# Kernel tuning notes

Hardware: AMD Instinct MI355X
Metric: run time of the kernel (lower is better)

The kernel has to match this reference:

```python
import jax, jax.numpy as jnp
import numpy as np

HIDDEN = 2048
NUM_HEADS = 16
HEAD_DIM = HIDDEN // NUM_HEADS
HARMONICS = 64


def _holo_params(key, in_features, out_features, harmonics):
    kb, kp = jax.random.split(key)
    basis = jax.random.normal(kb, (harmonics, in_features), dtype=jnp.float32)
    basis = basis / jnp.linalg.norm(basis, axis=1, keepdims=True)  # F.normalize(p=2, dim=1)
    phase = jax.random.normal(kp, (out_features, harmonics), dtype=jnp.float32) * 0.1
    amp = jnp.ones((out_features, harmonics), dtype=jnp.float32) / np.sqrt(harmonics).astype(np.float32)
    return basis, phase, amp


def setup_inputs() -> dict:
    key = jax.random.key(0)
    ks = jax.random.split(key, 5)
    hidden_states = jax.random.normal(ks[0], (2, 2048, HIDDEN), dtype=jnp.float32)
    inp = {"hidden_states": hidden_states}
    for name, k in zip(("q", "k", "v", "o"), ks[1:]):
        basis, phase, amp = _holo_params(k, HIDDEN, HIDDEN, HARMONICS)
        inp[f"basis_{name}"] = basis
        inp[f"phase_{name}"] = phase
        inp[f"amp_{name}"] = amp
    return inp


def _holo_linear(x, basis, phase, amp):
    # resonance: (B,S,H) = x @ basis^T; modulated-sum == resonance @ (amp*cos(phase))^T
    resonance = jnp.einsum('bsd,hd->bsh', x, basis)
    w = amp * jnp.cos(phase)  # (out, harmonics)
    return jnp.einsum('bsh,oh->bso', resonance, w)


def reference(hidden_states, basis_q, phase_q, amp_q, basis_k, phase_k, amp_k,
              basis_v, phase_v, amp_v, basis_o, phase_o, amp_o):
    bsz, seq_len, _ = hidden_states.shape
    q = _holo_linear(hidden_states, basis_q, phase_q, amp_q)
    k = _holo_linear(hidden_states, basis_k, phase_k, amp_k)
    v = _holo_linear(hidden_states, basis_v, phase_v, amp_v)
    # (B, H, S, Dh)
    q = q.reshape(bsz, seq_len, NUM_HEADS, HEAD_DIM).transpose(0, 2, 1, 3)
    k = k.reshape(bsz, seq_len, NUM_HEADS, HEAD_DIM).transpose(0, 2, 1, 3)
    v = v.reshape(bsz, seq_len, NUM_HEADS, HEAD_DIM).transpose(0, 2, 1, 3)
    scale = 1.0 / np.sqrt(HEAD_DIM).astype(np.float32)
    scores = jnp.einsum('bhqd,bhkd->bhqk', q, k) * scale
    attn = jax.nn.softmax(scores, axis=-1)
    out = jnp.einsum('bhqk,bhkd->bhqd', attn, v)
    out = out.transpose(0, 2, 1, 3).reshape(bsz, seq_len, HIDDEN)
    return _holo_linear(out, basis_o, phase_o, amp_o)
```

## Files before the change

### kernel.cpp

```cpp
#include <hip/hip_runtime.h>
#include <hip/hip_bf16.h>
#include <math.h>

#define HIDDEN 2048
#define HARM   64
#define NHEADS 16
#define HDIM   128
#define SEQ    2048
#define BATCH  2
#define ROWS   (BATCH*SEQ)
#define RN     (ROWS*HARM)
#define PN     ((size_t)ROWS*HIDDEN)

using bf16x8 = __attribute__((ext_vector_type(8))) short;
using f32x16 = __attribute__((ext_vector_type(16))) float;
using u32x2  = __attribute__((ext_vector_type(2))) unsigned;

#if defined(__has_builtin)
#if __has_builtin(__builtin_amdgcn_exp2f)
#define EXP2F(x) __builtin_amdgcn_exp2f(x)
#else
#define EXP2F(x) exp2f(x)
#endif
#else
#define EXP2F(x) exp2f(x)
#endif

#if defined(__has_builtin) && __has_builtin(__builtin_amdgcn_permlane32_swap)
__device__ inline void plane_swap_u(unsigned& a, unsigned& b) {
  u32x2 r = __builtin_amdgcn_permlane32_swap(a, b, false, false);
  a = r[0]; b = r[1];
}
__device__ inline void plane_swap_f(float& a, float& b) {
  union { float f; unsigned u; } ua, ub;
  ua.f = a; ub.f = b;
  u32x2 r = __builtin_amdgcn_permlane32_swap(ua.u, ub.u, false, false);
  ua.u = r[0]; ub.u = r[1];
  a = ua.f; b = ub.f;
}
#else
__device__ inline void plane_swap_u(unsigned& a, unsigned& b) {
  const bool hi = (threadIdx.x & 32) != 0;
  unsigned ax = (unsigned)__shfl_xor((int)a, 32);
  unsigned bx = (unsigned)__shfl_xor((int)b, 32);
  unsigned r0 = hi ? bx : a;
  unsigned r1 = hi ? b : ax;
  a = r0; b = r1;
}
__device__ inline void plane_swap_f(float& a, float& b) {
  const bool hi = (threadIdx.x & 32) != 0;
  float ax = __shfl_xor(a, 32);
  float bx = __shfl_xor(b, 32);
  float r0 = hi ? bx : a;
  float r1 = hi ? b : ax;
  a = r0; b = r1;
}
#endif

__device__ inline void split_bf(float a, ushort& hi, ushort& lo) {
  __hip_bfloat16 h = __float2bfloat16(a);
  float hf = __bfloat162float(h);
  __hip_bfloat16 l = __float2bfloat16(a - hf);
  union { __hip_bfloat16 b; ushort u; } c1, c2;
  c1.b = h; c2.b = l;
  hi = c1.u; lo = c2.u;
}

__global__ __launch_bounds__(256) void prep(
    const float* __restrict__ X,
    const float* __restrict__ pq, const float* __restrict__ aq,
    const float* __restrict__ pk, const float* __restrict__ ak,
    const float* __restrict__ pv, const float* __restrict__ av,
    const float* __restrict__ po, const float* __restrict__ ao,
    const float* __restrict__ bq, const float* __restrict__ bk,
    const float* __restrict__ bv, const float* __restrict__ bo,
    ushort* __restrict__ Xh, ushort* __restrict__ Xl,
    ushort* __restrict__ Wh, ushort* __restrict__ Wl,
    ushort* __restrict__ Bh, ushort* __restrict__ Bl) {
  const int bid = blockIdx.x;
  const int t = threadIdx.x;
  if (bid < 8192) {
    size_t i = ((size_t)bid * 256 + t) * 4;
    float4 v = *(const float4*)&X[i];
    ushort4 h, l;
    split_bf(v.x, h.x, l.x); split_bf(v.y, h.y, l.y);
    split_bf(v.z, h.z, l.z); split_bf(v.w, h.w, l.w);
    *(ushort4*)&Xh[i] = h;
    *(ushort4*)&Xl[i] = l;
  } else if (bid < 10240) {
    int i = (bid - 8192) * 256 + t;
    const int N = HIDDEN * HARM;
    int set = i / N, j = i - set * N;
    const float* p = (set == 0) ? pq : (set == 1) ? pk : (set == 2) ? pv : po;
    const float* a = (set == 0) ? aq : (set == 1) ? ak : (set == 2) ? av : ao;
    float wv = a[j] * cosf(p[j]);
    ushort h, l;
    split_bf(wv, h, l);
    size_t o = (size_t)set * N + j;
    Wh[o] = h; Wl[o] = l;
  } else {
    int idx = bid - 10240;
    int z = idx >> 7, xb = idx & 127;
    const float* S = (z == 0) ? bq : (z == 1) ? bk : (z == 2) ? bv : bo;
    size_t i = ((size_t)xb * 256 + t) * 4;
    float4 v = *(const float4*)&S[i];
    ushort4 h, l;
    split_bf(v.x, h.x, l.x); split_bf(v.y, h.y, l.y);
    split_bf(v.z, h.z, l.z); split_bf(v.w, h.w, l.w);
    size_t o = (size_t)z * HARM * HIDDEN + i;
    *(ushort4*)&Bh[o] = h;
    *(ushort4*)&Bl[o] = l;
  }
}

__global__ __launch_bounds__(256) void gemm_res(
    const ushort* __restrict__ Xh, const ushort* __restrict__ Xl,
    const ushort* __restrict__ Bh, const ushort* __restrict__ Bl,
    float* __restrict__ R0, float* __restrict__ R1, float* __restrict__ R2) {
  const int z = blockIdx.z;
  const ushort* Bhz = Bh + (size_t)z * HARM * HIDDEN;
  const ushort* Blz = Bl + (size_t)z * HARM * HIDDEN;
  float* Rp = (z == 0) ? R0 : (z == 1) ? R1 : R2;
  const int row0 = blockIdx.x * 64;
  const int kc = blockIdx.y;
  __shared__ __align__(16) ushort Xs[2][64][72];
  __shared__ __align__(16) ushort Bs[2][64][72];
  const int t = threadIdx.x;
  const int lane = t & 63, w = t >> 6;
  const int l31 = lane & 31, hh = lane >> 5;
  const int m0 = (w & 1) * 32, n0 = (w >> 1) * 32;
  const int srow = t >> 2;
  const int sc = (t & 3) * 16;
  f32x16 acc;
  #pragma unroll
  for (int j = 0; j < 16; ++j) acc[j] = 0.0f;

  const int kbase = kc * 512;
  for (int k0 = kbase; k0 < kbase + 512; k0 += 64) {
    const size_t xo = (size_t)(row0 + srow) * HIDDEN + k0 + sc;
    const size_t bo = (size_t)srow * HIDDEN + k0 + sc;
    *(uint4*)&Xs[0][srow][sc]     = *(const uint4*)&Xh[xo];
    *(uint4*)&Xs[0][srow][sc + 8] = *(const uint4*)&Xh[xo + 8];
    *(uint4*)&Xs[1][srow][sc]     = *(const uint4*)&Xl[xo];
    *(uint4*)&Xs[1][srow][sc + 8] = *(const uint4*)&Xl[xo + 8];
    *(uint4*)&Bs[0][srow][sc]     = *(const uint4*)&Bhz[bo];
    *(uint4*)&Bs[0][srow][sc + 8] = *(const uint4*)&Bhz[bo + 8];
    *(uint4*)&Bs[1][srow][sc]     = *(const uint4*)&Blz[bo];
    *(uint4*)&Bs[1][srow][sc + 8] = *(const uint4*)&Blz[bo + 8];
    __syncthreads();
    #pragma unroll
    for (int ks = 0; ks < 4; ++ks) {
      bf16x8 ah = *(const bf16x8*)&Xs[0][m0 + l31][ks * 16 + 8 * hh];
      bf16x8 al = *(const bf16x8*)&Xs[1][m0 + l31][ks * 16 + 8 * hh];
      bf16x8 bh = *(const bf16x8*)&Bs[0][n0 + l31][ks * 16 + 8 * hh];
      bf16x8 bl = *(const bf16x8*)&Bs[1][n0 + l31][ks * 16 + 8 * hh];
      acc = __builtin_amdgcn_mfma_f32_32x32x16_bf16(ah, bh, acc, 0, 0, 0);
      acc = __builtin_amdgcn_mfma_f32_32x32x16_bf16(al, bh, acc, 0, 0, 0);
      acc = __builtin_amdgcn_mfma_f32_32x32x16_bf16(ah, bl, acc, 0, 0, 0);
    }
    __syncthreads();
  }
  float* out = Rp + (size_t)kc * ROWS * HARM;
  #pragma unroll
  for (int r = 0; r < 16; ++r) {
    int mloc = (r & 3) + 8 * (r >> 2) + 4 * hh;
    out[(size_t)(row0 + m0 + mloc) * HARM + n0 + l31] = acc[r];
  }
}

__global__ __launch_bounds__(256) void reduce_r(
    const float* __restrict__ R0, const float* __restrict__ R1,
    const float* __restrict__ R2,
    ushort* __restrict__ H0, ushort* __restrict__ L0,
    ushort* __restrict__ H1, ushort* __restrict__ L1,
    ushort* __restrict__ H2, ushort* __restrict__ L2) {
  const int z = blockIdx.y;
  const float* Rp = (z == 0) ? R0 : (z == 1) ? R1 : R2;
  ushort* H = (z == 0) ? H0 : (z == 1) ? H1 : H2;
  ushort* L = (z == 0) ? L0 : (z == 1) ? L1 : L2;
  const size_t i = ((size_t)blockIdx.x * 256 + threadIdx.x) * 8;
  ushort4 h0, l0, h1, l1;
  #pragma unroll
  for (int half = 0; half < 2; ++half) {
    const size_t o = i + half * 4;
    float4 p0 = *(const float4*)&Rp[o];
    float4 p1 = *(const float4*)&Rp[RN + o];
    float4 p2 = *(const float4*)&Rp[2 * (size_t)RN + o];
    float4 p3 = *(const float4*)&Rp[3 * (size_t)RN + o];
    ushort4& hh = half ? h1 : h0;
    ushort4& ll = half ? l1 : l0;
    split_bf(p0.x + p1.x + p2.x + p3.x, hh.x, ll.x);
    split_bf(p0.y + p1.y + p2.y + p3.y, hh.y, ll.y);
    split_bf(p0.z + p1.z + p2.z + p3.z, hh.z, ll.z);
    split_bf(p0.w + p1.w + p2.w + p3.w, hh.w, ll.w);
  }
  *(ushort4*)&H[i] = h0; *(ushort4*)&H[i + 4] = h1;
  *(ushort4*)&L[i] = l0; *(ushort4*)&L[i + 4] = l1;
}

__global__ __launch_bounds__(256) void gemm_proj(
    const ushort* __restrict__ Rh0, const ushort* __restrict__ Rl0,
    const ushort* __restrict__ Rh1, const ushort* __restrict__ Rl1,
    const ushort* __restrict__ Rh2, const ushort* __restrict__ Rl2,
    const ushort* __restrict__ Wh, const ushort* __restrict__ Wl,
    ushort* __restrict__ P0, ushort* __restrict__ P1, ushort* __restrict__ Vt) {
  const int z = blockIdx.z;
  const ushort* Rh = (z == 0) ? Rh0 : (z == 1) ? Rh1 : Rh2;
  const ushort* Rl = (z == 0) ? Rl0 : (z == 1) ? Rl1 : Rl2;
  const ushort* Whz = Wh + (size_t)z * HIDDEN * HARM;
  const ushort* Wlz = Wl + (size_t)z * HIDDEN * HARM;
  const int row0 = blockIdx.x * 32;
  const int col0 = blockIdx.y * 128;
  __shared__ __align__(16) union PSM {
    struct { ushort Rs[2][32][72]; ushort Ws[2][128][72]; } s;
    ushort ct[128][36];
  } sm;
  const int t = threadIdx.x;
  const int lane = t & 63, w = t >> 6;
  const int l31 = lane & 31, hh = lane >> 5;
  {
    const int r = t >> 3, h0 = (t & 7) * 8;
    const size_t o = (size_t)(row0 + r) * HARM + h0;
    *(uint4*)&sm.s.Rs[0][r][h0] = *(const uint4*)&Rh[o];
    *(uint4*)&sm.s.Rs[1][r][h0] = *(const uint4*)&Rl[o];
  }
  #pragma unroll
  for (int i = 0; i < 4; ++i) {
    int idx = t + i * 256;
    int o = idx >> 3, c8 = (idx & 7) * 8;
    const size_t go = (size_t)(col0 + o) * HARM + c8;
    *(uint4*)&sm.s.Ws[0][o][c8] = *(const uint4*)&Whz[go];
    *(uint4*)&sm.s.Ws[1][o][c8] = *(const uint4*)&Wlz[go];
  }
  __syncthreads();
  const int n0 = w * 32;
  f32x16 acc;
  #pragma unroll
  for (int j = 0; j < 16; ++j) acc[j] = 0.0f;
  #pragma unroll
  for (int ks = 0; ks < 4; ++ks) {
    bf16x8 ah = *(const bf16x8*)&sm.s.Rs[0][l31][ks * 16 + 8 * hh];
    bf16x8 al = *(const bf16x8*)&sm.s.Rs[1][l31][ks * 16 + 8 * hh];
    bf16x8 bh = *(const bf16x8*)&sm.s.Ws[0][n0 + l31][ks * 16 + 8 * hh];
    bf16x8 bl = *(const bf16x8*)&sm.s.Ws[1][n0 + l31][ks * 16 + 8 * hh];
    acc = __builtin_amdgcn_mfma_f32_32x32x16_bf16(ah, bh, acc, 0, 0, 0);
    acc = __builtin_amdgcn_mfma_f32_32x32x16_bf16(al, bh, acc, 0, 0, 0);
    acc = __builtin_amdgcn_mfma_f32_32x32x16_bf16(ah, bl, acc, 0, 0, 0);
  }
  if (z < 2) {
    ushort* P = (z == 0) ? P0 : P1;
    #pragma unroll
    for (int r = 0; r < 16; ++r) {
      int mloc = (r & 3) + 8 * (r >> 2) + 4 * hh;
      union { __hip_bfloat16 b; ushort u; } cv;
      cv.b = __float2bfloat16(acc[r]);
      P[(size_t)(row0 + mloc) * HIDDEN + col0 + n0 + l31] = cv.u;
    }
  } else {
    __syncthreads();
    #pragma unroll
    for (int r = 0; r < 16; ++r) {
      int mloc = (r & 3) + 8 * (r >> 2) + 4 * hh;
      union { __hip_bfloat16 b; ushort u; } cv;
      cv.b = __float2bfloat16(acc[r]);
      sm.ct[n0 + l31][mloc] = cv.u;
    }
    __syncthreads();
    if (t < 128) {
      const int batch = row0 >> 11;
      const int tok0 = row0 & 2047;
      ushort* dst = Vt + (size_t)batch * SEQ * HIDDEN +
                    (size_t)(col0 + t) * SEQ + tok0;
      #pragma unroll
      for (int j = 0; j < 4; ++j)
        *(uint4*)&dst[j * 8] = *(const uint4*)&sm.ct[t][j * 8];
    }
  }
}

__global__ __launch_bounds__(256) void gemm_proj_f32(
    const ushort* __restrict__ Rh, const ushort* __restrict__ Rl,
    const ushort* __restrict__ Whz, const ushort* __restrict__ Wlz,
    float* __restrict__ P) {
  const int row0 = blockIdx.x * 32;
  const int col0 = blockIdx.y * 128;
  __shared__ __align__(16) ushort Rs[2][32][72];
  __shared__ __align__(16) ushort Ws[2][128][72];
  const int t = threadIdx.x;
  const int lane = t & 63, w = t >> 6;
  const int l31 = lane & 31, hh = lane >> 5;
  {
    const int r = t >> 3, h0 = (t & 7) * 8;
    const size_t o = (size_t)(row0 + r) * HARM + h0;
    *(uint4*)&Rs[0][r][h0] = *(const uint4*)&Rh[o];
    *(uint4*)&Rs[1][r][h0] = *(const uint4*)&Rl[o];
  }
  #pragma unroll
  for (int i = 0; i < 4; ++i) {
    int idx = t + i * 256;
    int o = idx >> 3, c8 = (idx & 7) * 8;
    const size_t go = (size_t)(col0 + o) * HARM + c8;
    *(uint4*)&Ws[0][o][c8] = *(const uint4*)&Whz[go];
    *(uint4*)&Ws[1][o][c8] = *(const uint4*)&Wlz[go];
  }
  __syncthreads();
  const int n0 = w * 32;
  f32x16 acc;
  #pragma unroll
  for (int j = 0; j < 16; ++j) acc[j] = 0.0f;
  #pragma unroll
  for (int ks = 0; ks < 4; ++ks) {
    bf16x8 ah = *(const bf16x8*)&Rs[0][l31][ks * 16 + 8 * hh];
    bf16x8 al = *(const bf16x8*)&Rs[1][l31][ks * 16 + 8 * hh];
    bf16x8 bh = *(const bf16x8*)&Ws[0][n0 + l31][ks * 16 + 8 * hh];
    bf16x8 bl = *(const bf16x8*)&Ws[1][n0 + l31][ks * 16 + 8 * hh];
    acc = __builtin_amdgcn_mfma_f32_32x32x16_bf16(ah, bh, acc, 0, 0, 0);
    acc = __builtin_amdgcn_mfma_f32_32x32x16_bf16(al, bh, acc, 0, 0, 0);
    acc = __builtin_amdgcn_mfma_f32_32x32x16_bf16(ah, bl, acc, 0, 0, 0);
  }
  #pragma unroll
  for (int r = 0; r < 16; ++r) {
    int mloc = (r & 3) + 8 * (r >> 2) + 4 * hh;
    P[(size_t)(row0 + mloc) * HIDDEN + col0 + n0 + l31] = acc[r];
  }
}

#define BQ 128
#define BK 64
#define KSTR 136
#define VSTR 72

__device__ inline unsigned pkbf(float a, float b) {
  __hip_bfloat162 h2 = __float22bfloat162_rn(make_float2(a, b));
  union { __hip_bfloat162 h; unsigned u; } cv; cv.h = h2; return cv.u;
}

__global__ __launch_bounds__(256, 2) void attn_mfma(
    const ushort* __restrict__ Qg, const ushort* __restrict__ Kg,
    const ushort* __restrict__ Vt, ushort* __restrict__ Oh,
    ushort* __restrict__ Ol) {
  __shared__ __align__(16) union SM {
    ushort q[BQ][KSTR];
    struct { ushort k[BK][KSTR]; ushort v[HDIM][VSTR]; } kv[2];
  } sm;
  const int t = threadIdx.x;
  const int bh = blockIdx.x & 31;
  const int qt = blockIdx.x >> 5;
  const int b = bh >> 4, h = bh & 15;
  const int q0 = qt * BQ;
  const int lane = t & 63;
  const int w = t >> 6;
  const int l31 = lane & 31;
  const int hh = lane >> 5;
  const float SC2 = 0.08838834764831845f * 1.4426950408889634f;

  const int sk_key = t >> 4;
  const int sk_d0 = (t & 15) * 8;
  const int sv_d = t >> 3;
  const int sv_k = (t & 7) * 8;
  const size_t kbase = ((size_t)(b * SEQ)) * HIDDEN + h * HDIM;
  const size_t vbase = ((size_t)(b * SEQ + h * HDIM)) * SEQ;

  {
    const size_t gbase = ((size_t)(b * SEQ + q0)) * HIDDEN + h * HDIM;
    for (int p = 0; p < 8; ++p) {
      int row = p * 16 + sk_key;
      uint4 v = *(const uint4*)&Qg[gbase + (size_t)row * HIDDEN + sk_d0];
      *(uint4*)&sm.q[row][sk_d0] = v;
    }
  }
  __syncthreads();
  bf16x8 Qf[8];
  {
    const int qrow = w * 32 + l31;
    #pragma unroll
    for (int ks = 0; ks < 8; ++ks)
      Qf[ks] = *(const bf16x8*)&sm.q[qrow][ks * 16 + 8 * hh];
  }
  __syncthreads();

  float mrow = -1e30f, lsum = 0.0f;
  f32x16 Ot[4];
  #pragma unroll
  for (int i = 0; i < 4; ++i)
    #pragma unroll
    for (int j = 0; j < 16; ++j) Ot[i][j] = 0.0f;
  f32x16 Zv;
  #pragma unroll
  for (int j = 0; j < 16; ++j) Zv[j] = 0.0f;

  uint4 kp[4], vp[4];
  {
    const size_t gb = kbase;
    #pragma unroll
    for (int p = 0; p < 4; ++p)
      kp[p] = *(const uint4*)&Kg[gb + (size_t)(p * 16 + sk_key) * HIDDEN + sk_d0];
    #pragma unroll
    for (int p = 0; p < 4; ++p)
      vp[p] = *(const uint4*)&Vt[vbase + (size_t)(p * 32 + sv_d) * SEQ + sv_k];
    #pragma unroll
    for (int p = 0; p < 4; ++p)
      *(uint4*)&sm.kv[0].k[p * 16 + sk_key][sk_d0] = kp[p];
    #pragma unroll
    for (int p = 0; p < 4; ++p)
      *(uint4*)&sm.kv[0].v[p * 32 + sv_d][sv_k] = vp[p];
  }
  __syncthreads();

  for (int ci = 0; ci < 32; ++ci) {
    {
      const int cn = (ci < 31) ? ci + 1 : 31;
      const size_t gb = kbase + (size_t)(cn * BK) * HIDDEN;
      #pragma unroll
      for (int p = 0; p < 4; ++p)
        kp[p] = *(const uint4*)&Kg[gb + (size_t)(p * 16 + sk_key) * HIDDEN + sk_d0];
      const size_t vb = vbase + cn * BK;
      #pragma unroll
      for (int p = 0; p < 4; ++p)
        vp[p] = *(const uint4*)&Vt[vb + (size_t)(p * 32 + sv_d) * SEQ + sv_k];
    }
    const int cb = ci & 1;

    f32x16 C0, C1;
    {
      bf16x8 a0 = *(const bf16x8*)&sm.kv[cb].k[l31][8 * hh];
      bf16x8 a1 = *(const bf16x8*)&sm.kv[cb].k[32 + l31][8 * hh];
      __builtin_amdgcn_s_setprio(1);
      C0 = __builtin_amdgcn_mfma_f32_32x32x16_bf16(a0, Qf[0], Zv, 0, 0, 0);
      C1 = __builtin_amdgcn_mfma_f32_32x32x16_bf16(a1, Qf[0], Zv, 0, 0, 0);
      #pragma unroll
      for (int ks = 1; ks < 8; ++ks) {
        bf16x8 b0 = *(const bf16x8*)&sm.kv[cb].k[l31][ks * 16 + 8 * hh];
        bf16x8 b1 = *(const bf16x8*)&sm.kv[cb].k[32 + l31][ks * 16 + 8 * hh];
        C0 = __builtin_amdgcn_mfma_f32_32x32x16_bf16(b0, Qf[ks], C0, 0, 0, 0);
        C1 = __builtin_amdgcn_mfma_f32_32x32x16_bf16(b1, Qf[ks], C1, 0, 0, 0);
      }
      __builtin_amdgcn_s_setprio(0);
    }

    float m01[16];
    #pragma unroll
    for (int j = 0; j < 16; ++j) m01[j] = fmaxf(C0[j], C1[j]);
    float x0 = fmaxf(fmaxf(m01[0], m01[1]), m01[2]);
    float x1 = fmaxf(fmaxf(m01[3], m01[4]), m01[5]);
    float x2 = fmaxf(fmaxf(m01[6], m01[7]), m01[8]);
    float x3 = fmaxf(fmaxf(m01[9], m01[10]), m01[11]);
    float x4 = fmaxf(fmaxf(m01[12], m01[13]), m01[14]);
    float mxr = fmaxf(fmaxf(fmaxf(x0, x1), fmaxf(x2, x3)), fmaxf(x4, m01[15]));
    {
      float u = mxr, v2 = mxr;
      plane_swap_f(u, v2);
      mxr = fmaxf(u, v2);
    }

    const float mg = mxr * SC2;
    if (__any(mg > mrow)) {
      const float mnew = fmaxf(mrow, mg);
      const float alpha = EXP2F(mrow - mnew);
      lsum *= alpha;
      #pragma unroll
      for (int i = 0; i < 4; ++i)
        #pragma unroll
        for (int j = 0; j < 16; ++j) Ot[i][j] *= alpha;
      mrow = mnew;
    }
    float s0 = 0.0f, s1 = 0.0f, s2 = 0.0f, s3 = 0.0f;
    #pragma unroll
    for (int j = 0; j < 16; ++j) {
      float e0 = EXP2F(fmaf(C0[j], SC2, -mrow));
      float e1 = EXP2F(fmaf(C1[j], SC2, -mrow));
      C0[j] = e0; C1[j] = e1;
      if (j & 1) { s2 += e0; s3 += e1; } else { s0 += e0; s1 += e1; }
    }
    lsum += (s0 + s1) + (s2 + s3);

    #pragma unroll
    for (int st = 0; st < 4; ++st) {
      const int eb = 8 * (st & 1);
      unsigned A0, A1, B0, B1;
      if (st < 2) {
        A0 = pkbf(C0[eb + 0], C0[eb + 1]); A1 = pkbf(C0[eb + 2], C0[eb + 3]);
        B0 = pkbf(C0[eb + 4], C0[eb + 5]); B1 = pkbf(C0[eb + 6], C0[eb + 7]);
      } else {
        A0 = pkbf(C1[eb + 0], C1[eb + 1]); A1 = pkbf(C1[eb + 2], C1[eb + 3]);
        B0 = pkbf(C1[eb + 4], C1[eb + 5]); B1 = pkbf(C1[eb + 6], C1[eb + 7]);
      }
      plane_swap_u(A0, B0);
      plane_swap_u(A1, B1);
      union { unsigned u[4]; bf16x8 v; } cv;
      cv.u[0] = A0; cv.u[1] = A1; cv.u[2] = B0; cv.u[3] = B1;
      __builtin_amdgcn_s_setprio(1);
      #pragma unroll
      for (int mt = 0; mt < 4; ++mt) {
        bf16x8 a2 = *(const bf16x8*)&sm.kv[cb].v[mt * 32 + l31][st * 16 + 8 * hh];
        Ot[mt] = __builtin_amdgcn_mfma_f32_32x32x16_bf16(a2, cv.v, Ot[mt], 0, 0, 0);
      }
      __builtin_amdgcn_s_setprio(0);
    }

    {
      const int nb = cb ^ 1;
      #pragma unroll
      for (int p = 0; p < 4; ++p)
        *(uint4*)&sm.kv[nb].k[p * 16 + sk_key][sk_d0] = kp[p];
      #pragma unroll
      for (int p = 0; p < 4; ++p)
        *(uint4*)&sm.kv[nb].v[p * 32 + sv_d][sv_k] = vp[p];
    }
    __syncthreads();
  }

  {
    float u = lsum, v2 = lsum;
    plane_swap_f(u, v2);
    lsum = u + v2;
  }
  const float inv = 1.0f / lsum;
  const int qrow = q0 + w * 32 + l31;
  const size_t ob = ((size_t)(b * SEQ + qrow)) * HIDDEN + h * HDIM;
  #pragma unroll
  for (int mt = 0; mt < 4; ++mt)
    #pragma unroll
    for (int g = 0; g < 4; ++g) {
      ushort4 hs, ls;
      split_bf(Ot[mt][4 * g + 0] * inv, hs.x, ls.x);
      split_bf(Ot[mt][4 * g + 1] * inv, hs.y, ls.y);
      split_bf(Ot[mt][4 * g + 2] * inv, hs.z, ls.z);
      split_bf(Ot[mt][4 * g + 3] * inv, hs.w, ls.w);
      const size_t off = ob + mt * 32 + 8 * g + 4 * hh;
      *(ushort4*)&Oh[off] = hs;
      *(ushort4*)&Ol[off] = ls;
    }
}

extern "C" void kernel_launch(void* const* d_in, const int* in_sizes, int n_in,
                              void* d_out, int out_size, void* d_ws, size_t ws_size,
                              hipStream_t stream) {
  (void)in_sizes; (void)n_in; (void)out_size; (void)ws_size;
  const float* X       = (const float*)d_in[0];
  const float* basis_q = (const float*)d_in[1];
  const float* phase_q = (const float*)d_in[2];
  const float* amp_q   = (const float*)d_in[3];
  const float* basis_k = (const float*)d_in[4];
  const float* phase_k = (const float*)d_in[5];
  const float* amp_k   = (const float*)d_in[6];
  const float* basis_v = (const float*)d_in[7];
  const float* phase_v = (const float*)d_in[8];
  const float* amp_v   = (const float*)d_in[9];
  const float* basis_o = (const float*)d_in[10];
  const float* phase_o = (const float*)d_in[11];
  const float* amp_o   = (const float*)d_in[12];

  const size_t WN = (size_t)HIDDEN * HARM;

  char* p = (char*)d_ws;
  ushort* Xhi = (ushort*)p; p += PN * 2;
  ushort* Xlo = (ushort*)p; p += PN * 2;
  ushort* Bhi = (ushort*)p; p += 4 * WN * 2;
  ushort* Blo = (ushort*)p; p += 4 * WN * 2;
  ushort* Whi = (ushort*)p; p += 4 * WN * 2;
  ushort* Wlo = (ushort*)p; p += 4 * WN * 2;
  float* Rqp = (float*)p; p += (size_t)4 * RN * 4;
  float* Rkp = (float*)p; p += (size_t)4 * RN * 4;
  float* Rvp = (float*)p; p += (size_t)4 * RN * 4;
  float* Rop = (float*)p; p += (size_t)4 * RN * 4;
  __hip_bfloat16* Qb = (__hip_bfloat16*)p; p += PN * 2;
  __hip_bfloat16* Kb = (__hip_bfloat16*)p; p += PN * 2;
  __hip_bfloat16* VtB = (__hip_bfloat16*)p; p += PN * 2;
  ushort* AOh = (ushort*)p; p += PN * 2;
  ushort* AOl = (ushort*)p; p += PN * 2;
  ushort* Rqh = (ushort*)p; p += RN * 2;
  ushort* Rql = (ushort*)p; p += RN * 2;
  ushort* Rkh = (ushort*)p; p += RN * 2;
  ushort* Rkl = (ushort*)p; p += RN * 2;
  ushort* Rvh = (ushort*)p; p += RN * 2;
  ushort* Rvl = (ushort*)p; p += RN * 2;
  ushort* Roh = (ushort*)p; p += RN * 2;
  ushort* Rol = (ushort*)p; p += RN * 2;
  float* out = (float*)d_out;

  prep<<<10752, 256, 0, stream>>>(X,
                                  phase_q, amp_q, phase_k, amp_k,
                                  phase_v, amp_v, phase_o, amp_o,
                                  basis_q, basis_k, basis_v, basis_o,
                                  Xhi, Xlo, Whi, Wlo, Bhi, Blo);

  gemm_res<<<dim3(64, 4, 3), 256, 0, stream>>>(Xhi, Xlo, Bhi, Blo, Rqp, Rkp, Rvp);

  reduce_r<<<dim3(RN / 2048, 3), 256, 0, stream>>>(
      Rqp, Rkp, Rvp, Rqh, Rql, Rkh, Rkl, Rvh, Rvl);

  gemm_proj<<<dim3(128, 16, 3), 256, 0, stream>>>(
      Rqh, Rql, Rkh, Rkl, Rvh, Rvl, Whi, Wlo,
      (ushort*)Qb, (ushort*)Kb, (ushort*)VtB);

  attn_mfma<<<dim3((SEQ / BQ) * 32), 256, 0, stream>>>(
      (const ushort*)Qb, (const ushort*)Kb, (const ushort*)VtB, AOh, AOl);

  gemm_res<<<dim3(64, 4, 1), 256, 0, stream>>>(
      AOh, AOl, Bhi + 3 * WN, Blo + 3 * WN, Rop, Rop, Rop);

  reduce_r<<<dim3(RN / 2048, 1), 256, 0, stream>>>(
      Rop, Rop, Rop, Roh, Rol, Roh, Rol, Roh, Rol);

  gemm_proj_f32<<<dim3(128, 16), 256, 0, stream>>>(
      Roh, Rol, Whi + 3 * WN, Wlo + 3 * WN, out);
}
```

Before: 259.9 us.

## Use 128-row tiles with 8-way split-K for QKV resonance GEMM

Adds a gemm_res128 kernel in which each block covers 128 rows and all 64 harmonics, with each wave computing two 32x32 tiles. The basis tile is loaded once per block and reused across more rows, and the K split becomes 8 chunks of 256, so the grid keeps 768 blocks. The reduce kernel now takes a runtime partial count, sized for the larger QKV partial buffers. The cost is twice the partial-sum traffic through the reduction and a larger workspace.

```diff
diff --git a/kernel.cpp b/kernel.cpp
--- a/kernel.cpp
+++ b/kernel.cpp
@@ -113,6 +113,73 @@
   }
 }
 
+__global__ __launch_bounds__(256) void gemm_res128(
+    const ushort* __restrict__ Xh, const ushort* __restrict__ Xl,
+    const ushort* __restrict__ Bh, const ushort* __restrict__ Bl,
+    float* __restrict__ R0, float* __restrict__ R1, float* __restrict__ R2) {
+  const int z = blockIdx.z;
+  const ushort* Bhz = Bh + (size_t)z * HARM * HIDDEN;
+  const ushort* Blz = Bl + (size_t)z * HARM * HIDDEN;
+  float* Rp = (z == 0) ? R0 : (z == 1) ? R1 : R2;
+  const int row0 = blockIdx.x * 128;
+  const int kc = blockIdx.y;
+  __shared__ __align__(16) ushort Xs[2][128][72];
+  __shared__ __align__(16) ushort Bs[2][64][72];
+  const int t = threadIdx.x;
+  const int lane = t & 63, w = t >> 6;
+  const int l31 = lane & 31, hh = lane >> 5;
+  const int xrow = t >> 1;
+  const int xc = (t & 1) * 32;
+  const int brow = t >> 2;
+  const int bc = (t & 3) * 16;
+  f32x16 acc0, acc1;
+  #pragma unroll
+  for (int j = 0; j < 16; ++j) { acc0[j] = 0.0f; acc1[j] = 0.0f; }
+
+  const int kbase = kc * 256;
+  for (int k0 = kbase; k0 < kbase + 256; k0 += 64) {
+    const size_t xo = (size_t)(row0 + xrow) * HIDDEN + k0 + xc;
+    const size_t bo = (size_t)brow * HIDDEN + k0 + bc;
+    *(uint4*)&Xs[0][xrow][xc]      = *(const uint4*)&Xh[xo];
+    *(uint4*)&Xs[0][xrow][xc + 8]  = *(const uint4*)&Xh[xo + 8];
+    *(uint4*)&Xs[0][xrow][xc + 16] = *(const uint4*)&Xh[xo + 16];
+    *(uint4*)&Xs[0][xrow][xc + 24] = *(const uint4*)&Xh[xo + 24];
+    *(uint4*)&Xs[1][xrow][xc]      = *(const uint4*)&Xl[xo];
+    *(uint4*)&Xs[1][xrow][xc + 8]  = *(const uint4*)&Xl[xo + 8];
+    *(uint4*)&Xs[1][xrow][xc + 16] = *(const uint4*)&Xl[xo + 16];
+    *(uint4*)&Xs[1][xrow][xc + 24] = *(const uint4*)&Xl[xo + 24];
+    *(uint4*)&Bs[0][brow][bc]     = *(const uint4*)&Bhz[bo];
+    *(uint4*)&Bs[0][brow][bc + 8] = *(const uint4*)&Bhz[bo + 8];
+    *(uint4*)&Bs[1][brow][bc]     = *(const uint4*)&Blz[bo];
+    *(uint4*)&Bs[1][brow][bc + 8] = *(const uint4*)&Blz[bo + 8];
+    __syncthreads();
+    #pragma unroll
+    for (int ks = 0; ks < 4; ++ks) {
+      bf16x8 ah  = *(const bf16x8*)&Xs[0][w * 32 + l31][ks * 16 + 8 * hh];
+      bf16x8 al  = *(const bf16x8*)&Xs[1][w * 32 + l31][ks * 16 + 8 * hh];
+      bf16x8 bh0 = *(const bf16x8*)&Bs[0][l31][ks * 16 + 8 * hh];
+      bf16x8 bl0 = *(const bf16x8*)&Bs[1][l31][ks * 16 + 8 * hh];
+      bf16x8 bh1 = *(const bf16x8*)&Bs[0][32 + l31][ks * 16 + 8 * hh];
+      bf16x8 bl1 = *(const bf16x8*)&Bs[1][32 + l31][ks * 16 + 8 * hh];
+      acc0 = __builtin_amdgcn_mfma_f32_32x32x16_bf16(ah, bh0, acc0, 0, 0, 0);
+      acc0 = __builtin_amdgcn_mfma_f32_32x32x16_bf16(al, bh0, acc0, 0, 0, 0);
+      acc0 = __builtin_amdgcn_mfma_f32_32x32x16_bf16(ah, bl0, acc0, 0, 0, 0);
+      acc1 = __builtin_amdgcn_mfma_f32_32x32x16_bf16(ah, bh1, acc1, 0, 0, 0);
+      acc1 = __builtin_amdgcn_mfma_f32_32x32x16_bf16(al, bh1, acc1, 0, 0, 0);
+      acc1 = __builtin_amdgcn_mfma_f32_32x32x16_bf16(ah, bl1, acc1, 0, 0, 0);
+    }
+    __syncthreads();
+  }
+  float* out = Rp + (size_t)kc * RN;
+  #pragma unroll
+  for (int r = 0; r < 16; ++r) {
+    int mloc = (r & 3) + 8 * (r >> 2) + 4 * hh;
+    const size_t ro = (size_t)(row0 + w * 32 + mloc) * HARM;
+    out[ro + l31] = acc0[r];
+    out[ro + 32 + l31] = acc1[r];
+  }
+}
+
 __global__ __launch_bounds__(256) void gemm_res(
     const ushort* __restrict__ Xh, const ushort* __restrict__ Xl,
     const ushort* __restrict__ Bh, const ushort* __restrict__ Bl,
@@ -170,7 +237,7 @@
 
 __global__ __launch_bounds__(256) void reduce_r(
     const float* __restrict__ R0, const float* __restrict__ R1,
-    const float* __restrict__ R2,
+    const float* __restrict__ R2, int np,
     ushort* __restrict__ H0, ushort* __restrict__ L0,
     ushort* __restrict__ H1, ushort* __restrict__ L1,
     ushort* __restrict__ H2, ushort* __restrict__ L2) {
@@ -183,16 +250,17 @@
   #pragma unroll
   for (int half = 0; half < 2; ++half) {
     const size_t o = i + half * 4;
-    float4 p0 = *(const float4*)&Rp[o];
-    float4 p1 = *(const float4*)&Rp[RN + o];
-    float4 p2 = *(const float4*)&Rp[2 * (size_t)RN + o];
-    float4 p3 = *(const float4*)&Rp[3 * (size_t)RN + o];
+    float4 s = *(const float4*)&Rp[o];
+    for (int pp = 1; pp < np; ++pp) {
+      float4 q = *(const float4*)&Rp[(size_t)pp * RN + o];
+      s.x += q.x; s.y += q.y; s.z += q.z; s.w += q.w;
+    }
     ushort4& hh = half ? h1 : h0;
     ushort4& ll = half ? l1 : l0;
-    split_bf(p0.x + p1.x + p2.x + p3.x, hh.x, ll.x);
-    split_bf(p0.y + p1.y + p2.y + p3.y, hh.y, ll.y);
-    split_bf(p0.z + p1.z + p2.z + p3.z, hh.z, ll.z);
-    split_bf(p0.w + p1.w + p2.w + p3.w, hh.w, ll.w);
+    split_bf(s.x, hh.x, ll.x);
+    split_bf(s.y, hh.y, ll.y);
+    split_bf(s.z, hh.z, ll.z);
+    split_bf(s.w, hh.w, ll.w);
   }
   *(ushort4*)&H[i] = h0; *(ushort4*)&H[i + 4] = h1;
   *(ushort4*)&L[i] = l0; *(ushort4*)&L[i + 4] = l1;
@@ -560,9 +628,9 @@
   ushort* Blo = (ushort*)p; p += 4 * WN * 2;
   ushort* Whi = (ushort*)p; p += 4 * WN * 2;
   ushort* Wlo = (ushort*)p; p += 4 * WN * 2;
-  float* Rqp = (float*)p; p += (size_t)4 * RN * 4;
-  float* Rkp = (float*)p; p += (size_t)4 * RN * 4;
-  float* Rvp = (float*)p; p += (size_t)4 * RN * 4;
+  float* Rqp = (float*)p; p += (size_t)8 * RN * 4;
+  float* Rkp = (float*)p; p += (size_t)8 * RN * 4;
+  float* Rvp = (float*)p; p += (size_t)8 * RN * 4;
   float* Rop = (float*)p; p += (size_t)4 * RN * 4;
   __hip_bfloat16* Qb = (__hip_bfloat16*)p; p += PN * 2;
   __hip_bfloat16* Kb = (__hip_bfloat16*)p; p += PN * 2;
@@ -585,10 +653,11 @@
                                   basis_q, basis_k, basis_v, basis_o,
                                   Xhi, Xlo, Whi, Wlo, Bhi, Blo);
 
-  gemm_res<<<dim3(64, 4, 3), 256, 0, stream>>>(Xhi, Xlo, Bhi, Blo, Rqp, Rkp, Rvp);
+  gemm_res128<<<dim3(32, 8, 3), 256, 0, stream>>>(
+      Xhi, Xlo, Bhi, Blo, Rqp, Rkp, Rvp);
 
   reduce_r<<<dim3(RN / 2048, 3), 256, 0, stream>>>(
-      Rqp, Rkp, Rvp, Rqh, Rql, Rkh, Rkl, Rvh, Rvl);
+      Rqp, Rkp, Rvp, 8, Rqh, Rql, Rkh, Rkl, Rvh, Rvl);
 
   gemm_proj<<<dim3(128, 16, 3), 256, 0, stream>>>(
       Rqh, Rql, Rkh, Rkl, Rvh, Rvl, Whi, Wlo,
@@ -601,7 +670,7 @@
       AOh, AOl, Bhi + 3 * WN, Blo + 3 * WN, Rop, Rop, Rop);
 
   reduce_r<<<dim3(RN / 2048, 1), 256, 0, stream>>>(
-      Rop, Rop, Rop, Roh, Rol, Roh, Rol, Roh, Rol);
+      Rop, Rop, Rop, 4, Roh, Rol, Roh, Rol, Roh, Rol);
 
   gemm_proj_f32<<<dim3(128, 16), 256, 0, stream>>>(
       Roh, Rol, Whi + 3 * WN, Wlo + 3 * WN, out);
```

Measured after the change: 269.2 us. 1.04x slower.
